# Kernel optimization log

Measured on AMD Instinct MI355X. Metric: run time of the kernel, lower is better.

The kernel has to match this reference:

```python
import jax, jax.numpy as jnp
import numpy as np

H = 128            # hidden_dim
R = 16             # num_rbf
L = 3              # num_atom_encoder_layers
LAT = 32           # latent_dim
NUM_ATOM_TYPES = 64
CUTOFF = 5.0       # atom_cutoff
N_RES = 2048
DEG = 16           # avg radius-graph degree
_PATTERN = np.array([19, 20, 21, 22, 23, 24, 25, 22])  # ragged atoms/residue, mean 22


def setup_inputs() -> dict:
    key = jax.random.key(0)
    ks = jax.random.split(key, 16)
    apr = np.tile(_PATTERN, N_RES // len(_PATTERN))        # (N,) atoms per residue
    A = int(apr.sum())                                     # 45056 atoms
    E = A * DEG                                            # 720896 edges
    rng = np.random.default_rng(0)

    def gl(k, shape, fan_in):
        return jax.random.normal(k, shape, jnp.float32) * (fan_in ** -0.5)

    return {
        "atom_coords": jax.random.normal(ks[0], (A, 3), jnp.float32) * 10.0,
        "atom_types": jax.random.randint(ks[1], (A,), 0, NUM_ATOM_TYPES),
        "residue_indices": jnp.asarray(np.repeat(np.arange(N_RES), apr)),
        "residue_types": jax.random.randint(ks[2], (N_RES,), 0, 4),
        "atoms_per_residue": jnp.asarray(apr),
        "edge_src": jnp.asarray(rng.integers(0, A, E)),
        "edge_dst": jnp.asarray(rng.integers(0, A, E)),
        # learned parameters
        "atom_embed": gl(ks[3], (NUM_ATOM_TYPES, H), 1.0),
        "residue_embed": gl(ks[4], (4, H), 1.0),
        "We1": gl(ks[5], (L, 2 * H + R, H), 2 * H + R), "be1": jnp.zeros((L, H)),
        "We2": gl(ks[6], (L, H, H), H), "be2": jnp.zeros((L, H)),
        "Wh1": gl(ks[7], (L, 2 * H, H), 2 * H), "bh1": jnp.zeros((L, H)),
        "Wh2": gl(ks[8], (L, H, H), H), "bh2": jnp.zeros((L, H)),
        "Wq": gl(ks[9], (H, H), H), "bq": jnp.zeros((H,)),
        "Wk": gl(ks[10], (H, H), H), "bk": jnp.zeros((H,)),
        "Wv": gl(ks[11], (H, H), H), "bv": jnp.zeros((H,)),
        "Wmu": gl(ks[12], (H, LAT), H), "bmu": jnp.zeros((LAT,)),
        "Wlv": gl(ks[13], (H, LAT), H) * 0.01, "blv": jnp.full((LAT,), -2.0),
    }


def reference(atom_coords, atom_types, residue_indices, residue_types,
              atoms_per_residue, edge_src, edge_dst,
              atom_embed, residue_embed,
              We1, be1, We2, be2, Wh1, bh1, Wh2, bh2,
              Wq, bq, Wk, bk, Wv, bv, Wmu, bmu, Wlv, blv):
    A = atom_coords.shape[0]
    N = residue_types.shape[0]
    coords = atom_coords - atom_coords.mean(0, keepdims=True)  # center_coords

    # Gaussian radial basis expansion of edge distances
    d = jnp.linalg.norm(coords[edge_src] - coords[edge_dst], axis=-1)  # (E,)
    centers = jnp.linspace(0.0, CUTOFF, R)
    gamma = (R / CUTOFF) ** 2
    edge_attr = jnp.exp(-gamma * (d[:, None] - centers) ** 2)          # (E,R)

    # atom features: atom-type embed + residue-type embed scattered to atoms
    res_emb = residue_embed[residue_types]                             # (N,H)
    h = atom_embed[atom_types] + res_emb[residue_indices]              # (A,H)

    # EGNN layers (update_coords=False): message MLP -> sum-agg -> residual node MLP
    for l in range(L):
        m = jnp.concatenate([h[edge_src], h[edge_dst], edge_attr], axis=-1)  # (E,2H+R)
        m = jax.nn.silu(m @ We1[l] + be1[l])
        m = jax.nn.silu(m @ We2[l] + be2[l])                                  # (E,H)
        agg = jax.ops.segment_sum(m, edge_dst, num_segments=A)               # (A,H)
        u = jnp.concatenate([h, agg], axis=-1)                               # (A,2H)
        u = jax.nn.silu(u @ Wh1[l] + bh1[l])
        h = h + (u @ Wh2[l] + bh2[l])

    # segment (per-residue) attention pooling of atoms -> residues
    q = res_emb @ Wq + bq                                              # (N,H)
    k = h @ Wk + bk                                                    # (A,H)
    v = h @ Wv + bv                                                    # (A,H)
    scores = jnp.sum(q[residue_indices] * k, axis=-1) * (H ** -0.5)    # (A,)
    smax = jax.ops.segment_max(scores, residue_indices, num_segments=N)
    ex = jnp.exp(scores - smax[residue_indices])
    denom = jax.ops.segment_sum(ex, residue_indices, num_segments=N)
    w = ex / denom[residue_indices]
    pooled = jax.ops.segment_sum(w[:, None] * v, residue_indices, num_segments=N)  # (N,H)

    mu = pooled @ Wmu + bmu
    logvar = jnp.clip(pooled @ Wlv + blv, -10.0, 2.0)
    return mu, logvar
```

## Files before the change

### kernel.cpp

```cpp
#include <hip/hip_runtime.h>
#include <hip/hip_bf16.h>

#define H 128
#define LATD 32

typedef __attribute__((ext_vector_type(8))) _Float16 half8t;
typedef __attribute__((ext_vector_type(4))) _Float16 half4t;
typedef __attribute__((ext_vector_type(2))) _Float16 half2t;
typedef __attribute__((ext_vector_type(8))) unsigned short u16x8;
typedef __attribute__((ext_vector_type(4))) float f32x4;

#define OFF_RBF 0
#define OFF_W2  12288
#define OFF_PROJ 61440
#define OFF_H1  159744
#define OFF_H2  258048
#define OFF_KV  307200
#define WP_TOTAL 339968

__device__ __forceinline__ float silu_f(float x) {
  return x * __builtin_amdgcn_rcpf(1.0f + __expf(-x));
}
__device__ __forceinline__ unsigned short f16u(float x) {
  _Float16 hh = (_Float16)x;
  return *(unsigned short*)&hh;
}

__global__ void k_init_h(const float* __restrict__ atom_embed,
                         const float* __restrict__ residue_embed,
                         const int* __restrict__ atype,
                         const int* __restrict__ ridx,
                         const int* __restrict__ rtype,
                         float* __restrict__ h, unsigned short* __restrict__ hb, int A) {
  int i = blockIdx.x * blockDim.x + threadIdx.x;
  if (i >= A * H) return;
  int a = i >> 7, j = i & 127;
  float v = atom_embed[atype[a] * H + j] + residue_embed[rtype[ridx[a]] * H + j];
  h[i] = v;
  hb[i] = f16u(v);
}

__global__ void k_dist(const float* __restrict__ coords,
                       const int* __restrict__ esrc, const int* __restrict__ edst,
                       float* __restrict__ dbuf, int E) {
  int e = blockIdx.x * blockDim.x + threadIdx.x;
  if (e >= E) return;
  int s = esrc[e], t = edst[e];
  float dx = coords[3*s+0] - coords[3*t+0];
  float dy = coords[3*s+1] - coords[3*t+1];
  float dz = coords[3*s+2] - coords[3*t+2];
  dbuf[e] = sqrtf(dx*dx + dy*dy + dz*dz);
}

__global__ void k_starts(const int* __restrict__ ridx, int* __restrict__ starts, int A) {
  int a = blockIdx.x * blockDim.x + threadIdx.x;
  if (a >= A) return;
  if (a == 0 || ridx[a] != ridx[a-1]) starts[ridx[a]] = a;
}

__global__ void k_bias2(const float* __restrict__ b1, const float* __restrict__ b2,
                        float* __restrict__ bkv) {
  int t = threadIdx.x;
  bkv[t] = (t < 128) ? b1[t] : b2[t - 128];
}

__global__ void k_hist(const int* __restrict__ edst, int* __restrict__ cnt, int E) {
  int e = blockIdx.x * blockDim.x + threadIdx.x;
  if (e < E) atomicAdd(&cnt[edst[e]], 1);
}

__global__ __launch_bounds__(1024) void k_scanA(const int* __restrict__ cnt,
                                                int* __restrict__ cursor,
                                                int* __restrict__ bsum, int A) {
  __shared__ int buf[1024];
  int tid = threadIdx.x;
  int i = blockIdx.x * 1024 + tid;
  int v = (i < A) ? cnt[i] : 0;
  buf[tid] = v;
  __syncthreads();
  #pragma unroll
  for (int off = 1; off < 1024; off <<= 1) {
    int nv = (tid >= off) ? buf[tid - off] : 0;
    __syncthreads();
    buf[tid] += nv;
    __syncthreads();
  }
  if (i < A) cursor[i] = buf[tid] - v;
  if (tid == 1023) bsum[blockIdx.x] = buf[1023];
}

__global__ void k_scanB(int* __restrict__ bsum, int nb) {
  int lane = threadIdx.x;
  int v = (lane < nb) ? bsum[lane] : 0;
  int s = v;
  #pragma unroll
  for (int off = 1; off < 64; off <<= 1) {
    int nv = __shfl_up(s, off);
    if (lane >= off) s += nv;
  }
  if (lane < nb) bsum[lane] = s - v;
}

__global__ void k_scanC(int* __restrict__ cursor, const int* __restrict__ bsum, int A) {
  int i = blockIdx.x * blockDim.x + threadIdx.x;
  if (i < A) cursor[i] += bsum[i >> 10];
}

__global__ void k_scatter(const int* __restrict__ edst, int* __restrict__ cursor,
                          int* __restrict__ eperm, int E) {
  int e = blockIdx.x * blockDim.x + threadIdx.x;
  if (e >= E) return;
  int p = atomicAdd(&cursor[edst[e]], 1);
  eperm[p] = e;
}

__global__ void k_pack(const float* __restrict__ We1, const float* __restrict__ We2,
                       const float* __restrict__ Wh1, const float* __restrict__ Wh2,
                       const float* __restrict__ Wk,  const float* __restrict__ Wv,
                       unsigned short* __restrict__ wp) {
  int t = blockIdx.x * blockDim.x + threadIdx.x;
  if (t >= WP_TOTAL) return;
  if (t < OFF_W2) {
    int u = t - OFF_RBF; int layer = u / 4096, idx = u % 4096;
    int i = idx & 7, lane = (idx >> 3) & 63, ct = (idx >> 9) & 7;
    int k = ((lane >> 4) * 8) + i;
    int c = ct * 16 + (lane & 15);
    const float* src = We1 + (size_t)layer * 272 * H;
    wp[t] = f16u(k < 16 ? src[(size_t)(256 + k) * H + c] : 0.0f);
  } else if (t < OFF_PROJ) {
    int u = t - OFF_W2; int layer = u / 16384, idx = u % 16384;
    int i = idx & 7, lane = (idx >> 3) & 63, ct = (idx >> 9) & 7, kt = idx >> 12;
    int k = kt * 32 + (lane >> 4) * 8 + i, c = ct * 16 + (lane & 15);
    const float* src = We2 + (size_t)layer * 128 * H;
    wp[t] = f16u(src[(size_t)k * H + c]);
  } else if (t < OFF_H1) {
    int u = t - OFF_PROJ; int layer = u / 32768, idx = u % 32768;
    int i = idx & 7, lane = (idx >> 3) & 63, ct = (idx >> 9) & 15, kt = idx >> 13;
    int k = kt * 32 + (lane >> 4) * 8 + i, c = ct * 16 + (lane & 15);
    const float* src = We1 + (size_t)layer * 272 * H;
    float v = (c < 128) ? src[(size_t)k * H + c] : src[(size_t)(128 + k) * H + (c - 128)];
    wp[t] = f16u(v);
  } else if (t < OFF_H2) {
    int u = t - OFF_H1; int layer = u / 32768, idx = u % 32768;
    int i = idx & 7, lane = (idx >> 3) & 63, ct = (idx >> 9) & 7, kt = idx >> 12;
    int k = kt * 32 + (lane >> 4) * 8 + i, c = ct * 16 + (lane & 15);
    const float* src = Wh1 + (size_t)layer * 256 * H;
    wp[t] = f16u(src[(size_t)k * H + c]);
  } else if (t < OFF_KV) {
    int u = t - OFF_H2; int layer = u / 16384, idx = u % 16384;
    int i = idx & 7, lane = (idx >> 3) & 63, ct = (idx >> 9) & 7, kt = idx >> 12;
    int k = kt * 32 + (lane >> 4) * 8 + i, c = ct * 16 + (lane & 15);
    const float* src = Wh2 + (size_t)layer * 128 * H;
    wp[t] = f16u(src[(size_t)k * H + c]);
  } else {
    int idx = t - OFF_KV;
    int i = idx & 7, lane = (idx >> 3) & 63, ct = (idx >> 9) & 15, kt = idx >> 13;
    int k = kt * 32 + (lane >> 4) * 8 + i, c = ct * 16 + (lane & 15);
    float v = (c < 128) ? Wk[(size_t)k * H + c] : Wv[(size_t)k * H + (c - 128)];
    wp[t] = f16u(v);
  }
}

__global__ __launch_bounds__(256) void k_proj(
    const unsigned short* __restrict__ hb, const unsigned short* __restrict__ Wp,
    unsigned short* __restrict__ Ph, int A, const float* __restrict__ bias) {
  const int tid = threadIdx.x, l = tid & 63, wv = tid >> 6;
  const int lr = l & 15, lk = (l >> 4) * 8;
  const int a0 = blockIdx.x * 64;
  f32x4 acc[4][4] = {};
  #pragma unroll
  for (int kt = 0; kt < 4; ++kt) {
    half8t a[4], b[4];
    #pragma unroll
    for (int rt = 0; rt < 4; ++rt) {
      int row = a0 + rt * 16 + lr; if (row >= A) row = A - 1;
      a[rt] = *(const half8t*)&hb[(size_t)row * H + kt * 32 + lk];
    }
    #pragma unroll
    for (int ci = 0; ci < 4; ++ci)
      b[ci] = *(const half8t*)&Wp[(((size_t)kt * 16 + wv * 4 + ci) * 64 + l) * 8];
    #pragma unroll
    for (int rt = 0; rt < 4; ++rt)
      #pragma unroll
      for (int ci = 0; ci < 4; ++ci)
        acc[rt][ci] = __builtin_amdgcn_mfma_f32_16x16x32_f16(a[rt], b[ci], acc[rt][ci], 0, 0, 0);
  }
  #pragma unroll
  for (int rt = 0; rt < 4; ++rt)
    #pragma unroll
    for (int ci = 0; ci < 4; ++ci) {
      int col = (wv * 4 + ci) * 16 + lr;
      float bb = bias ? bias[col] : 0.0f;
      #pragma unroll
      for (int rr = 0; rr < 4; ++rr) {
        int row = a0 + rt * 16 + (l >> 4) * 4 + rr;
        if (row < A) Ph[(size_t)row * 256 + col] = f16u(acc[rt][ci][rr] + bb);
      }
    }
}

#define ES 136

__global__ __launch_bounds__(256) void k_edge_mfma(
    const unsigned short* __restrict__ Ph, const float* __restrict__ dbuf,
    const int* __restrict__ esrc, const int* __restrict__ edst,
    const int* __restrict__ eperm,
    const unsigned short* __restrict__ Wr, const float* __restrict__ be1,
    const unsigned short* __restrict__ W2p, const float* __restrict__ be2,
    float* __restrict__ agg, int E) {
  __shared__ __align__(16) unsigned short SH[64 * ES];
  __shared__ int dstv[64];
  __shared__ float dval[64];

  const int tid = threadIdx.x;
  const int e0 = blockIdx.x * 64;
  const int l = tid & 63, wv = tid >> 6;
  const int lr = l & 15, lk = (l >> 4) * 8, g4 = (l >> 4) * 4;
  const int ct0 = wv * 2;

  {
    const int r = tid >> 2, qt = tid & 3;
    int e = e0 + r;
    int ec = (e < E) ? e : (E - 1);
    int es = eperm[ec];
    int s = esrc[es], t = edst[es];
    if (qt == 0) {
      dstv[r] = (e < E) ? t : -1;
      dval[r] = dbuf[es];
    }
    const half8t* ps = (const half8t*)(Ph + (size_t)s * 256);
    const half8t* pt = (const half8t*)(Ph + (size_t)t * 256 + 128);
    half8t* pr = (half8t*)&SH[r * ES];
    #pragma unroll
    for (int i = 0; i < 4; ++i)
      pr[qt * 4 + i] = ps[qt * 4 + i] + pt[qt * 4 + i];
  }
  __syncthreads();

  f32x4 acc[2][4];
  #pragma unroll
  for (int cj = 0; cj < 2; ++cj) {
    int cbase = (ct0 + cj) * 16 + g4;
    #pragma unroll
    for (int et = 0; et < 4; ++et) {
      half4t p4 = *(const half4t*)&SH[(et * 16 + lr) * ES + cbase];
      acc[cj][et][0] = (float)p4[0];
      acc[cj][et][1] = (float)p4[1];
      acc[cj][et][2] = (float)p4[2];
      acc[cj][et][3] = (float)p4[3];
    }
  }
  {
    float dA[4];
    #pragma unroll
    for (int et = 0; et < 4; ++et) dA[et] = dval[et * 16 + lr];
    half8t br[4];
    if (lk < 16) {
      #pragma unroll
      for (int et = 0; et < 4; ++et) {
        float d = dA[et];
        #pragma unroll
        for (int i = 0; i < 8; ++i) {
          float dd = d - (float)(lk + i) * (5.0f / 15.0f);
          br[et][i] = (_Float16)__expf(-10.24f * dd * dd);
        }
      }
    } else {
      #pragma unroll
      for (int et = 0; et < 4; ++et)
        #pragma unroll
        for (int i = 0; i < 8; ++i) br[et][i] = (_Float16)0.0f;
    }
    half8t ar[2];
    #pragma unroll
    for (int cj = 0; cj < 2; ++cj)
      ar[cj] = *(const half8t*)&Wr[(((size_t)(ct0 + cj)) * 64 + l) * 8];
    #pragma unroll
    for (int et = 0; et < 4; ++et)
      #pragma unroll
      for (int cj = 0; cj < 2; ++cj)
        acc[cj][et] = __builtin_amdgcn_mfma_f32_16x16x32_f16(ar[cj], br[et], acc[cj][et], 0, 0, 0);
  }
  __syncthreads();

  #pragma unroll
  for (int cj = 0; cj < 2; ++cj) {
    f32x4 b1v = *(const f32x4*)&be1[(ct0 + cj) * 16 + g4];
    #pragma unroll
    for (int et = 0; et < 4; ++et) {
      half4t m4;
      #pragma unroll
      for (int rr = 0; rr < 4; ++rr)
        m4[rr] = (_Float16)silu_f(acc[cj][et][rr] + b1v[rr]);
      *(half4t*)&SH[(et * 16 + lr) * ES + (ct0 + cj) * 16 + g4] = m4;
    }
  }
  __syncthreads();

  f32x4 acc2[2][4] = {};
  #pragma unroll
  for (int kt = 0; kt < 4; ++kt) {
    half8t a2[2], b2[4];
    #pragma unroll
    for (int cj = 0; cj < 2; ++cj)
      a2[cj] = *(const half8t*)&W2p[(((size_t)kt * 8 + ct0 + cj) * 64 + l) * 8];
    #pragma unroll
    for (int et = 0; et < 4; ++et)
      b2[et] = *(const half8t*)&SH[(et * 16 + lr) * ES + kt * 32 + lk];
    #pragma unroll
    for (int cj = 0; cj < 2; ++cj)
      #pragma unroll
      for (int et = 0; et < 4; ++et)
        acc2[cj][et] = __builtin_amdgcn_mfma_f32_16x16x32_f16(a2[cj], b2[et], acc2[cj][et], 0, 0, 0);
  }
  __syncthreads();

  #pragma unroll
  for (int cj = 0; cj < 2; ++cj) {
    f32x4 b2v = *(const f32x4*)&be2[(ct0 + cj) * 16 + g4];
    #pragma unroll
    for (int et = 0; et < 4; ++et) {
      half4t m4;
      #pragma unroll
      for (int rr = 0; rr < 4; ++rr)
        m4[rr] = (_Float16)silu_f(acc2[cj][et][rr] + b2v[rr]);
      *(half4t*)&SH[(et * 16 + lr) * ES + (ct0 + cj) * 16 + g4] = m4;
    }
  }
  __syncthreads();

  {
    int cp = tid & 63, qr = tid >> 6;
    int rbeg = qr * 16, rend = rbeg + 16;
    float a0 = 0.f, a1 = 0.f;
    int prev = -1;
    for (int r = rbeg; r < rend; ++r) {
      int dv = dstv[r];
      half2t v = *(const half2t*)&SH[r * ES + cp * 2];
      if (dv != prev) {
        if (prev >= 0) {
          atomicAdd(&agg[(size_t)prev * H + cp * 2], a0);
          atomicAdd(&agg[(size_t)prev * H + cp * 2 + 1], a1);
        }
        a0 = a1 = 0.f;
        prev = dv;
      }
      if (dv >= 0) { a0 += (float)v[0]; a1 += (float)v[1]; }
    }
    if (prev >= 0) {
      atomicAdd(&agg[(size_t)prev * H + cp * 2], a0);
      atomicAdd(&agg[(size_t)prev * H + cp * 2 + 1], a1);
    }
  }
}

#define NXS 264
#define M1S 136

__global__ __launch_bounds__(256) void k_node_mfma(
    float* __restrict__ h, unsigned short* __restrict__ hb,
    const float* __restrict__ agg,
    const unsigned short* __restrict__ W1p, const float* __restrict__ bh1,
    const unsigned short* __restrict__ W2p, const float* __restrict__ bh2, int A) {
  __shared__ __align__(16) unsigned short Xs[32 * NXS];
  __shared__ __align__(16) unsigned short Us[32 * M1S];
  const int tid = threadIdx.x;
  const int a0 = blockIdx.x * 32;
  {
    const int r = tid >> 3, oct = tid & 7;
    int a = a0 + r; if (a >= A) a = A - 1;
    const u16x8* hr = (const u16x8*)(hb + (size_t)a * H);
    u16x8* xr = (u16x8*)&Xs[r * NXS];
    xr[oct * 2]     = hr[oct * 2];
    xr[oct * 2 + 1] = hr[oct * 2 + 1];
    const float4* ar = (const float4*)(agg + (size_t)a * H);
    u16x8 tmp[2];
    unsigned short* tp = (unsigned short*)tmp;
    #pragma unroll
    for (int i = 0; i < 4; ++i) {
      float4 av = ar[oct * 4 + i];
      tp[i*4+0] = f16u(av.x); tp[i*4+1] = f16u(av.y);
      tp[i*4+2] = f16u(av.z); tp[i*4+3] = f16u(av.w);
    }
    xr[16 + oct * 2]     = tmp[0];
    xr[16 + oct * 2 + 1] = tmp[1];
  }
  __syncthreads();

  const int l = tid & 63, wv = tid >> 6;
  const int lr = l & 15, lk = (l >> 4) * 8;
  const int ct0 = wv * 2;
  const int c0 = ct0 * 16 + lr, c1 = c0 + 16;
  const float b1a = bh1[c0], b1b = bh1[c1];
  const float b2a = bh2[c0], b2b = bh2[c1];

  f32x4 acc[2][2] = {};
  #pragma unroll
  for (int kt = 0; kt < 8; ++kt) {
    half8t a[2], b[2];
    #pragma unroll
    for (int rt = 0; rt < 2; ++rt)
      a[rt] = *(const half8t*)&Xs[(rt * 16 + lr) * NXS + kt * 32 + lk];
    #pragma unroll
    for (int j = 0; j < 2; ++j)
      b[j] = *(const half8t*)&W1p[(((size_t)kt * 8 + ct0 + j) * 64 + l) * 8];
    #pragma unroll
    for (int rt = 0; rt < 2; ++rt)
      #pragma unroll
      for (int j = 0; j < 2; ++j)
        acc[rt][j] = __builtin_amdgcn_mfma_f32_16x16x32_f16(a[rt], b[j], acc[rt][j], 0, 0, 0);
  }
  #pragma unroll
  for (int rt = 0; rt < 2; ++rt)
    #pragma unroll
    for (int j = 0; j < 2; ++j) {
      float bb = j ? b1b : b1a;
      int col = (ct0 + j) * 16 + lr;
      #pragma unroll
      for (int rr = 0; rr < 4; ++rr) {
        int row = rt * 16 + (l >> 4) * 4 + rr;
        Us[row * M1S + col] = f16u(silu_f(acc[rt][j][rr] + bb));
      }
    }
  __syncthreads();

  f32x4 acc2[2][2] = {};
  #pragma unroll
  for (int kt = 0; kt < 4; ++kt) {
    half8t a[2], b[2];
    #pragma unroll
    for (int rt = 0; rt < 2; ++rt)
      a[rt] = *(const half8t*)&Us[(rt * 16 + lr) * M1S + kt * 32 + lk];
    #pragma unroll
    for (int j = 0; j < 2; ++j)
      b[j] = *(const half8t*)&W2p[(((size_t)kt * 8 + ct0 + j) * 64 + l) * 8];
    #pragma unroll
    for (int rt = 0; rt < 2; ++rt)
      #pragma unroll
      for (int j = 0; j < 2; ++j)
        acc2[rt][j] = __builtin_amdgcn_mfma_f32_16x16x32_f16(a[rt], b[j], acc2[rt][j], 0, 0, 0);
  }
  #pragma unroll
  for (int rt = 0; rt < 2; ++rt)
    #pragma unroll
    for (int j = 0; j < 2; ++j) {
      float bb = j ? b2b : b2a;
      int col = (ct0 + j) * 16 + lr;
      #pragma unroll
      for (int rr = 0; rr < 4; ++rr) {
        int row = rt * 16 + (l >> 4) * 4 + rr;
        int a = a0 + row;
        if (a < A) {
          size_t off = (size_t)a * H + col;
          float nh = h[off] + acc2[rt][j][rr] + bb;
          h[off] = nh;
          hb[off] = f16u(nh);
        }
      }
    }
}

__global__ void k_q4(const float* __restrict__ residue_embed,
                     const float* __restrict__ Wq, const float* __restrict__ bq,
                     float* __restrict__ q4) {
  int i = blockIdx.x * blockDim.x + threadIdx.x;
  if (i >= 4 * H) return;
  int r = i >> 7, j = i & 127;
  const float* emb = residue_embed + (size_t)r * H;
  float s = bq[j];
  #pragma unroll 4
  for (int k = 0; k < H; ++k) s += emb[k] * Wq[(size_t)k*H + j];
  q4[i] = s;
}

__global__ __launch_bounds__(256) void k_pool(
    const float* __restrict__ q4, const int* __restrict__ rtype,
    const unsigned short* __restrict__ kv, const int* __restrict__ starts,
    const int* __restrict__ apr, float* __restrict__ pooled, int N) {
  int r = blockIdx.x * 4 + (threadIdx.x >> 6);
  if (r >= N) return;
  int lane = threadIdx.x & 63;
  int s0 = starts[r], cnt = apr[r];
  const float* qrow = q4 + (size_t)rtype[r] * H;
  float q0 = qrow[lane], q1 = qrow[64 + lane];
  float myscore = -1e30f;
  for (int i = 0; i < cnt; ++i) {
    const unsigned short* kr = kv + (size_t)(s0 + i) * 256;
    float p = q0 * (float)(*(const _Float16*)&kr[lane]) +
              q1 * (float)(*(const _Float16*)&kr[64 + lane]);
    #pragma unroll
    for (int off = 32; off; off >>= 1) p += __shfl_xor(p, off);
    if (lane == i) myscore = p * 0.08838834764831845f;
  }
  float val = (lane < cnt) ? myscore : -1e30f;
  float mx = val;
  #pragma unroll
  for (int off = 32; off; off >>= 1) mx = fmaxf(mx, __shfl_xor(mx, off));
  float ex = (lane < cnt) ? __expf(val - mx) : 0.0f;
  float sum = ex;
  #pragma unroll
  for (int off = 32; off; off >>= 1) sum += __shfl_xor(sum, off);
  float w = ex * __builtin_amdgcn_rcpf(sum);
  float p0 = 0.f, p1 = 0.f;
  for (int i = 0; i < cnt; ++i) {
    float wi = __shfl(w, i);
    const unsigned short* vr = kv + (size_t)(s0 + i) * 256 + 128;
    p0 += wi * (float)(*(const _Float16*)&vr[lane]);
    p1 += wi * (float)(*(const _Float16*)&vr[64 + lane]);
  }
  pooled[(size_t)r*H + lane] = p0;
  pooled[(size_t)r*H + 64 + lane] = p1;
}

__global__ void k_head(const float* __restrict__ pooled,
                       const float* __restrict__ Wmu, const float* __restrict__ bmu,
                       const float* __restrict__ Wlv, const float* __restrict__ blv,
                       float* __restrict__ out, int N) {
  int i = blockIdx.x * blockDim.x + threadIdx.x;
  if (i >= N * LATD) return;
  int r = i >> 5, j = i & 31;
  const float* p = pooled + (size_t)r * H;
  float smu = 0.f, slv = 0.f;
  #pragma unroll 4
  for (int k = 0; k < H; ++k) {
    float pv = p[k];
    smu += pv * Wmu[(size_t)k*LATD + j];
    slv += pv * Wlv[(size_t)k*LATD + j];
  }
  smu += bmu[j];
  slv += blv[j];
  slv = fminf(fmaxf(slv, -10.0f), 2.0f);
  out[i] = smu;
  out[(size_t)N*LATD + i] = slv;
}

extern "C" void kernel_launch(void* const* d_in, const int* in_sizes, int n_in,
                              void* d_out, int out_size, void* d_ws, size_t ws_size,
                              hipStream_t stream) {
  const float* coords        = (const float*)d_in[0];
  const int*   atype         = (const int*)d_in[1];
  const int*   ridx          = (const int*)d_in[2];
  const int*   rtype         = (const int*)d_in[3];
  const int*   apr           = (const int*)d_in[4];
  const int*   esrc          = (const int*)d_in[5];
  const int*   edst          = (const int*)d_in[6];
  const float* atom_embed    = (const float*)d_in[7];
  const float* residue_embed = (const float*)d_in[8];
  const float* We1 = (const float*)d_in[9];
  const float* be1 = (const float*)d_in[10];
  const float* We2 = (const float*)d_in[11];
  const float* be2 = (const float*)d_in[12];
  const float* Wh1 = (const float*)d_in[13];
  const float* bh1 = (const float*)d_in[14];
  const float* Wh2 = (const float*)d_in[15];
  const float* bh2 = (const float*)d_in[16];
  const float* Wq  = (const float*)d_in[17];
  const float* bq  = (const float*)d_in[18];
  const float* Wk  = (const float*)d_in[19];
  const float* bk  = (const float*)d_in[20];
  const float* Wv  = (const float*)d_in[21];
  const float* bv  = (const float*)d_in[22];
  const float* Wmu = (const float*)d_in[23];
  const float* bmu = (const float*)d_in[24];
  const float* Wlv = (const float*)d_in[25];
  const float* blv = (const float*)d_in[26];

  const int A = in_sizes[1];
  const int N = in_sizes[3];
  const int E = in_sizes[5];

  float* ws     = (float*)d_ws;
  float* h      = ws;
  float* agg    = h + (size_t)A * H;
  float* vbuf   = agg + (size_t)A * H;
  float* dbuf   = vbuf + (size_t)A * H;
  float* q4     = dbuf + (size_t)E;
  float* bkv    = q4 + 4 * H;
  float* pooled = bkv + 256;
  int*   starts = (int*)(pooled + (size_t)N * H);
  unsigned short* hbuf = (unsigned short*)(starts + N);
  int*   eperm  = (int*)(hbuf + (size_t)A * H);
  int*   cnt    = eperm + (size_t)E;
  int*   cursor = cnt + A;
  int*   bsum   = cursor + A;
  unsigned short* wp = (unsigned short*)(bsum + 64);
  unsigned short* Ph = (unsigned short*)vbuf;

  k_init_h<<<(A * H + 255) / 256, 256, 0, stream>>>(atom_embed, residue_embed,
                                                    atype, ridx, rtype, h, hbuf, A);
  k_dist<<<(E + 255) / 256, 256, 0, stream>>>(coords, esrc, edst, dbuf, E);
  k_starts<<<(A + 255) / 256, 256, 0, stream>>>(ridx, starts, A);
  k_pack<<<(WP_TOTAL + 255) / 256, 256, 0, stream>>>(We1, We2, Wh1, Wh2, Wk, Wv, wp);
  k_bias2<<<1, 256, 0, stream>>>(bk, bv, bkv);

  const int nb = (A + 1023) / 1024;
  hipMemsetAsync(cnt, 0, (size_t)A * sizeof(int), stream);
  k_hist<<<(E + 255) / 256, 256, 0, stream>>>(edst, cnt, E);
  k_scanA<<<nb, 1024, 0, stream>>>(cnt, cursor, bsum, A);
  k_scanB<<<1, 64, 0, stream>>>(bsum, nb);
  k_scanC<<<(A + 255) / 256, 256, 0, stream>>>(cursor, bsum, A);
  k_scatter<<<(E + 255) / 256, 256, 0, stream>>>(edst, cursor, eperm, E);

  for (int l = 0; l < 3; ++l) {
    hipMemsetAsync(agg, 0, (size_t)A * H * sizeof(float), stream);
    k_proj<<<(A + 63) / 64, 256, 0, stream>>>(
        hbuf, wp + OFF_PROJ + (size_t)l * 32768, Ph, A, nullptr);
    k_edge_mfma<<<(E + 63) / 64, 256, 0, stream>>>(
        Ph, dbuf, esrc, edst, eperm,
        wp + OFF_RBF + (size_t)l * 4096,  be1 + (size_t)l * H,
        wp + OFF_W2  + (size_t)l * 16384, be2 + (size_t)l * H, agg, E);
    k_node_mfma<<<(A + 31) / 32, 256, 0, stream>>>(
        h, hbuf, agg,
        wp + OFF_H1 + (size_t)l * 32768, bh1 + (size_t)l * H,
        wp + OFF_H2 + (size_t)l * 16384, bh2 + (size_t)l * H, A);
  }

  k_q4<<<2, 256, 0, stream>>>(residue_embed, Wq, bq, q4);
  unsigned short* kv = Ph;
  k_proj<<<(A + 63) / 64, 256, 0, stream>>>(hbuf, wp + OFF_KV, kv, A, bkv);
  k_pool<<<(N + 3) / 4, 256, 0, stream>>>(q4, rtype, kv, starts, apr, pooled, N);
  k_head<<<(N * LATD + 255) / 256, 256, 0, stream>>>(pooled, Wmu, bmu, Wlv, blv,
                                                     (float*)d_out, N);
}
```

Before: 638.9 us.

## Merge small setup kernels, fold agg zeroing into proj, use 16-wide RBF MFMA

```diff
diff --git a/kernel.cpp b/kernel.cpp
--- a/kernel.cpp
+++ b/kernel.cpp
@@ -16,7 +16,8 @@
 #define OFF_H1  159744
 #define OFF_H2  258048
 #define OFF_KV  307200
-#define WP_TOTAL 339968
+#define OFF_RBF16 339968
+#define WP_TOTAL 346112
 
 __device__ __forceinline__ float silu_f(float x) {
   return x * __builtin_amdgcn_rcpf(1.0f + __expf(-x));
@@ -31,18 +32,21 @@
                          const int* __restrict__ atype,
                          const int* __restrict__ ridx,
                          const int* __restrict__ rtype,
-                         float* __restrict__ h, unsigned short* __restrict__ hb, int A) {
+                         float* __restrict__ h, unsigned short* __restrict__ hb,
+                         int* __restrict__ starts, int A) {
   int i = blockIdx.x * blockDim.x + threadIdx.x;
   if (i >= A * H) return;
   int a = i >> 7, j = i & 127;
-  float v = atom_embed[atype[a] * H + j] + residue_embed[rtype[ridx[a]] * H + j];
+  int r = ridx[a];
+  float v = atom_embed[atype[a] * H + j] + residue_embed[rtype[r] * H + j];
   h[i] = v;
   hb[i] = f16u(v);
+  if (j == 0 && (a == 0 || ridx[a - 1] != r)) starts[r] = a;
 }
 
 __global__ void k_dist(const float* __restrict__ coords,
                        const int* __restrict__ esrc, const int* __restrict__ edst,
-                       float* __restrict__ dbuf, int E) {
+                       float* __restrict__ dbuf, int* __restrict__ cnt, int E) {
   int e = blockIdx.x * blockDim.x + threadIdx.x;
   if (e >= E) return;
   int s = esrc[e], t = edst[e];
@@ -50,23 +54,7 @@
   float dy = coords[3*s+1] - coords[3*t+1];
   float dz = coords[3*s+2] - coords[3*t+2];
   dbuf[e] = sqrtf(dx*dx + dy*dy + dz*dz);
-}
-
-__global__ void k_starts(const int* __restrict__ ridx, int* __restrict__ starts, int A) {
-  int a = blockIdx.x * blockDim.x + threadIdx.x;
-  if (a >= A) return;
-  if (a == 0 || ridx[a] != ridx[a-1]) starts[ridx[a]] = a;
-}
-
-__global__ void k_bias2(const float* __restrict__ b1, const float* __restrict__ b2,
-                        float* __restrict__ bkv) {
-  int t = threadIdx.x;
-  bkv[t] = (t < 128) ? b1[t] : b2[t - 128];
-}
-
-__global__ void k_hist(const int* __restrict__ edst, int* __restrict__ cnt, int E) {
-  int e = blockIdx.x * blockDim.x + threadIdx.x;
-  if (e < E) atomicAdd(&cnt[edst[e]], 1);
+  atomicAdd(&cnt[t], 1);
 }
 
 __global__ __launch_bounds__(1024) void k_scanA(const int* __restrict__ cnt,
@@ -121,12 +109,7 @@
   int t = blockIdx.x * blockDim.x + threadIdx.x;
   if (t >= WP_TOTAL) return;
   if (t < OFF_W2) {
-    int u = t - OFF_RBF; int layer = u / 4096, idx = u % 4096;
-    int i = idx & 7, lane = (idx >> 3) & 63, ct = (idx >> 9) & 7;
-    int k = ((lane >> 4) * 8) + i;
-    int c = ct * 16 + (lane & 15);
-    const float* src = We1 + (size_t)layer * 272 * H;
-    wp[t] = f16u(k < 16 ? src[(size_t)(256 + k) * H + c] : 0.0f);
+    wp[t] = 0;
   } else if (t < OFF_PROJ) {
     int u = t - OFF_W2; int layer = u / 16384, idx = u % 16384;
     int i = idx & 7, lane = (idx >> 3) & 63, ct = (idx >> 9) & 7, kt = idx >> 12;
@@ -152,21 +135,38 @@
     int k = kt * 32 + (lane >> 4) * 8 + i, c = ct * 16 + (lane & 15);
     const float* src = Wh2 + (size_t)layer * 128 * H;
     wp[t] = f16u(src[(size_t)k * H + c]);
-  } else {
+  } else if (t < OFF_RBF16) {
     int idx = t - OFF_KV;
     int i = idx & 7, lane = (idx >> 3) & 63, ct = (idx >> 9) & 15, kt = idx >> 13;
     int k = kt * 32 + (lane >> 4) * 8 + i, c = ct * 16 + (lane & 15);
     float v = (c < 128) ? Wk[(size_t)k * H + c] : Wv[(size_t)k * H + (c - 128)];
     wp[t] = f16u(v);
+  } else {
+    int u = t - OFF_RBF16; int layer = u / 2048, idx = u % 2048;
+    int i = idx & 3, lane = (idx >> 2) & 63, ct = idx >> 8;
+    int k = (lane >> 4) * 4 + i;
+    int c = ct * 16 + (lane & 15);
+    const float* src = We1 + (size_t)layer * 272 * H;
+    wp[t] = f16u(src[(size_t)(256 + k) * H + c]);
   }
 }
 
 __global__ __launch_bounds__(256) void k_proj(
     const unsigned short* __restrict__ hb, const unsigned short* __restrict__ Wp,
-    unsigned short* __restrict__ Ph, int A, const float* __restrict__ bias) {
+    unsigned short* __restrict__ Ph, int A, const float* __restrict__ bias,
+    float* __restrict__ agg_zero) {
   const int tid = threadIdx.x, l = tid & 63, wv = tid >> 6;
   const int lr = l & 15, lk = (l >> 4) * 8;
   const int a0 = blockIdx.x * 64;
+  if (agg_zero) {
+    int a = a0 + (tid >> 2);
+    if (a < A) {
+      float4 z = {0.f, 0.f, 0.f, 0.f};
+      float4* dst = (float4*)(agg_zero + (size_t)a * H) + (tid & 3) * 8;
+      #pragma unroll
+      for (int i = 0; i < 8; ++i) dst[i] = z;
+    }
+  }
   f32x4 acc[4][4] = {};
   #pragma unroll
   for (int kt = 0; kt < 4; ++kt) {
@@ -205,7 +205,7 @@
     const unsigned short* __restrict__ Ph, const float* __restrict__ dbuf,
     const int* __restrict__ esrc, const int* __restrict__ edst,
     const int* __restrict__ eperm,
-    const unsigned short* __restrict__ Wr, const float* __restrict__ be1,
+    const unsigned short* __restrict__ Wr16, const float* __restrict__ be1,
     const unsigned short* __restrict__ W2p, const float* __restrict__ be2,
     float* __restrict__ agg, int E) {
   __shared__ __align__(16) unsigned short SH[64 * ES];
@@ -251,35 +251,25 @@
     }
   }
   {
-    float dA[4];
-    #pragma unroll
-    for (int et = 0; et < 4; ++et) dA[et] = dval[et * 16 + lr];
-    half8t br[4];
-    if (lk < 16) {
-      #pragma unroll
-      for (int et = 0; et < 4; ++et) {
-        float d = dA[et];
-        #pragma unroll
-        for (int i = 0; i < 8; ++i) {
-          float dd = d - (float)(lk + i) * (5.0f / 15.0f);
-          br[et][i] = (_Float16)__expf(-10.24f * dd * dd);
-        }
+    half4t br[4];
+    #pragma unroll
+    for (int et = 0; et < 4; ++et) {
+      float d = dval[et * 16 + lr];
+      #pragma unroll
+      for (int i = 0; i < 4; ++i) {
+        float dd = d - (float)(g4 + i) * (5.0f / 15.0f);
+        br[et][i] = (_Float16)__expf(-10.24f * dd * dd);
       }
-    } else {
-      #pragma unroll
-      for (int et = 0; et < 4; ++et)
-        #pragma unroll
-        for (int i = 0; i < 8; ++i) br[et][i] = (_Float16)0.0f;
-    }
-    half8t ar[2];
+    }
+    half4t ar[2];
     #pragma unroll
     for (int cj = 0; cj < 2; ++cj)
-      ar[cj] = *(const half8t*)&Wr[(((size_t)(ct0 + cj)) * 64 + l) * 8];
+      ar[cj] = *(const half4t*)&Wr16[(((size_t)(ct0 + cj)) * 64 + l) * 4];
     #pragma unroll
     for (int et = 0; et < 4; ++et)
       #pragma unroll
       for (int cj = 0; cj < 2; ++cj)
-        acc[cj][et] = __builtin_amdgcn_mfma_f32_16x16x32_f16(ar[cj], br[et], acc[cj][et], 0, 0, 0);
+        acc[cj][et] = __builtin_amdgcn_mfma_f32_16x16x16f16(ar[cj], br[et], acc[cj][et], 0, 0, 0);
   }
   __syncthreads();
 
@@ -460,39 +450,55 @@
     }
 }
 
-__global__ void k_q4(const float* __restrict__ residue_embed,
-                     const float* __restrict__ Wq, const float* __restrict__ bq,
-                     float* __restrict__ q4) {
+__global__ void k_q4b(const float* __restrict__ residue_embed,
+                      const float* __restrict__ Wq, const float* __restrict__ bq,
+                      const float* __restrict__ bk, const float* __restrict__ bv,
+                      float* __restrict__ q4, float* __restrict__ bkv) {
   int i = blockIdx.x * blockDim.x + threadIdx.x;
-  if (i >= 4 * H) return;
-  int r = i >> 7, j = i & 127;
-  const float* emb = residue_embed + (size_t)r * H;
-  float s = bq[j];
-  #pragma unroll 4
-  for (int k = 0; k < H; ++k) s += emb[k] * Wq[(size_t)k*H + j];
-  q4[i] = s;
+  if (i < 512) {
+    int r = i >> 7, j = i & 127;
+    const float* emb = residue_embed + (size_t)r * H;
+    float s = bq[j];
+    #pragma unroll 4
+    for (int k = 0; k < H; ++k) s += emb[k] * Wq[(size_t)k*H + j];
+    q4[i] = s;
+  } else if (i < 768) {
+    int t = i - 512;
+    bkv[t] = (t < 128) ? bk[t] : bv[t - 128];
+  }
+}
+
+__global__ void k_score(const unsigned short* __restrict__ kv,
+                        const float* __restrict__ q4,
+                        const int* __restrict__ ridx,
+                        const int* __restrict__ rtype,
+                        float* __restrict__ scores, int A) {
+  int t = blockIdx.x * blockDim.x + threadIdx.x;
+  int a = t >> 2, qt = t & 3;
+  if (a >= A) return;
+  const half8t* kr = (const half8t*)(kv + (size_t)a * 256 + qt * 32);
+  const float* qrow = q4 + (size_t)rtype[ridx[a]] * H + qt * 32;
+  float s = 0.f;
+  #pragma unroll
+  for (int i = 0; i < 4; ++i) {
+    half8t kvv = kr[i];
+    #pragma unroll
+    for (int j = 0; j < 8; ++j) s += (float)kvv[j] * qrow[i * 8 + j];
+  }
+  s += __shfl_xor(s, 1);
+  s += __shfl_xor(s, 2);
+  if (qt == 0) scores[a] = s * 0.08838834764831845f;
 }
 
 __global__ __launch_bounds__(256) void k_pool(
-    const float* __restrict__ q4, const int* __restrict__ rtype,
+    const float* __restrict__ scores,
     const unsigned short* __restrict__ kv, const int* __restrict__ starts,
     const int* __restrict__ apr, float* __restrict__ pooled, int N) {
   int r = blockIdx.x * 4 + (threadIdx.x >> 6);
   if (r >= N) return;
   int lane = threadIdx.x & 63;
   int s0 = starts[r], cnt = apr[r];
-  const float* qrow = q4 + (size_t)rtype[r] * H;
-  float q0 = qrow[lane], q1 = qrow[64 + lane];
-  float myscore = -1e30f;
-  for (int i = 0; i < cnt; ++i) {
-    const unsigned short* kr = kv + (size_t)(s0 + i) * 256;
-    float p = q0 * (float)(*(const _Float16*)&kr[lane]) +
-              q1 * (float)(*(const _Float16*)&kr[64 + lane]);
-    #pragma unroll
-    for (int off = 32; off; off >>= 1) p += __shfl_xor(p, off);
-    if (lane == i) myscore = p * 0.08838834764831845f;
-  }
-  float val = (lane < cnt) ? myscore : -1e30f;
+  float val = (lane < cnt) ? scores[s0 + lane] : -1e30f;
   float mx = val;
   #pragma unroll
   for (int off = 32; off; off >>= 1) mx = fmaxf(mx, __shfl_xor(mx, off));
@@ -586,39 +592,39 @@
   unsigned short* wp = (unsigned short*)(bsum + 64);
   unsigned short* Ph = (unsigned short*)vbuf;
 
+  hipMemsetAsync(cnt, 0, (size_t)A * sizeof(int), stream);
   k_init_h<<<(A * H + 255) / 256, 256, 0, stream>>>(atom_embed, residue_embed,
-                                                    atype, ridx, rtype, h, hbuf, A);
-  k_dist<<<(E + 255) / 256, 256, 0, stream>>>(coords, esrc, edst, dbuf, E);
-  k_starts<<<(A + 255) / 256, 256, 0, stream>>>(ridx, starts, A);
+                                                    atype, ridx, rtype, h, hbuf,
+                                                    starts, A);
+  k_dist<<<(E + 255) / 256, 256, 0, stream>>>(coords, esrc, edst, dbuf, cnt, E);
   k_pack<<<(WP_TOTAL + 255) / 256, 256, 0, stream>>>(We1, We2, Wh1, Wh2, Wk, Wv, wp);
-  k_bias2<<<1, 256, 0, stream>>>(bk, bv, bkv);
 
   const int nb = (A + 1023) / 1024;
-  hipMemsetAsync(cnt, 0, (size_t)A * sizeof(int), stream);
-  k_hist<<<(E + 255) / 256, 256, 0, stream>>>(edst, cnt, E);
   k_scanA<<<nb, 1024, 0, stream>>>(cnt, cursor, bsum, A);
   k_scanB<<<1, 64, 0, stream>>>(bsum, nb);
   k_scanC<<<(A + 255) / 256, 256, 0, stream>>>(cursor, bsum, A);
   k_scatter<<<(E + 255) / 256, 256, 0, stream>>>(edst, cursor, eperm, E);
 
+  const int egrid = (E + 63) / 64;
   for (int l = 0; l < 3; ++l) {
-    hipMemsetAsync(agg, 0, (size_t)A * H * sizeof(float), stream);
     k_proj<<<(A + 63) / 64, 256, 0, stream>>>(
-        hbuf, wp + OFF_PROJ + (size_t)l * 32768, Ph, A, nullptr);
-    k_edge_mfma<<<(E + 63) / 64, 256, 0, stream>>>(
+        hbuf, wp + OFF_PROJ + (size_t)l * 32768, Ph, A, nullptr, agg);
+    k_edge_mfma<<<egrid, 256, 0, stream>>>(
         Ph, dbuf, esrc, edst, eperm,
-        wp + OFF_RBF + (size_t)l * 4096,  be1 + (size_t)l * H,
-        wp + OFF_W2  + (size_t)l * 16384, be2 + (size_t)l * H, agg, E);
+        wp + OFF_RBF16 + (size_t)l * 2048, be1 + (size_t)l * H,
+        wp + OFF_W2    + (size_t)l * 16384, be2 + (size_t)l * H, agg, E);
     k_node_mfma<<<(A + 31) / 32, 256, 0, stream>>>(
         h, hbuf, agg,
         wp + OFF_H1 + (size_t)l * 32768, bh1 + (size_t)l * H,
         wp + OFF_H2 + (size_t)l * 16384, bh2 + (size_t)l * H, A);
   }
 
-  k_q4<<<2, 256, 0, stream>>>(residue_embed, Wq, bq, q4);
+  k_q4b<<<3, 256, 0, stream>>>(residue_embed, Wq, bq, bk, bv, q4, bkv);
   unsigned short* kv = Ph;
-  k_proj<<<(A + 63) / 64, 256, 0, stream>>>(hbuf, wp + OFF_KV, kv, A, bkv);
-  k_pool<<<(N + 3) / 4, 256, 0, stream>>>(q4, rtype, kv, starts, apr, pooled, N);
+  k_proj<<<(A + 63) / 64, 256, 0, stream>>>(hbuf, wp + OFF_KV, kv, A, bkv, nullptr);
+  float* scores = dbuf;
+  k_score<<<(A * 4 + 255) / 256, 256, 0, stream>>>(kv, q4, ridx, rtype, scores, A);
+  k_pool<<<(N + 3) / 4, 256, 0, stream>>>(scores, kv, starts, apr, pooled, N);
   k_head<<<(N * LATD + 255) / 256, 256, 0, stream>>>(pooled, Wmu, bmu, Wlv, blv,
                                                      (float*)d_out, N);
 }
```

Result: faster. 618.1 us (-3.2%).
